# Performance work log

Measured on AMD Instinct MI355X. Metric: run time of the kernel, lower is better.

## Reference

```python
import jax, jax.numpy as jnp
import numpy as np

EMBED = 512
HEADS = 8
HD = EMBED // HEADS  # 64
NCLS = 1
WSIZE = 32
DIL = 2
WIN_LEN = 2 * WSIZE + 1  # 65


def setup_inputs() -> dict:
    key = jax.random.key(0)
    ks = jax.random.split(key, 5)
    B, S = 2, NCLS + 2048
    return {
        "x": jax.random.normal(ks[0], (B, S, EMBED), dtype=jnp.float32),
        "qkv_w": jax.random.normal(ks[1], (3 * EMBED, EMBED), dtype=jnp.float32) * 0.02,
        "qkv_b": jax.random.normal(ks[2], (3 * EMBED,), dtype=jnp.float32) * 0.02,
        "out_w": jax.random.normal(ks[3], (EMBED, EMBED), dtype=jnp.float32) * 0.02,
        "out_b": jax.random.normal(ks[4], (EMBED,), dtype=jnp.float32) * 0.02,
    }


def reference(x, qkv_w, qkv_b, out_w, out_b):
    B, S, E = x.shape
    P = S - NCLS  # patch_len
    scale = HD ** -0.5

    qkv = (x @ qkv_w.T + qkv_b).reshape(B, S, 3, HEADS, HD)
    qkv = qkv.transpose(2, 0, 3, 1, 4)  # (3, B, H, S, d)
    q, k, v = qkv[0], qkv[1], qkv[2]

    q_cls, k_cls, v_cls = q[:, :, :NCLS], k[:, :, :NCLS], v[:, :, :NCLS]
    q_p, k_p, v_p = q[:, :, NCLS:], k[:, :, NCLS:], v[:, :, NCLS:]

    # CLS queries: full attention over all S keys
    s_cls = jnp.einsum('bhqd,bhkd->bhqk', q_cls, k) * scale
    cls_out = jnp.einsum('bhqk,bhkd->bhqd', jax.nn.softmax(s_cls, axis=-1), v)

    # Patch queries: CLS keys + dilated local window
    pad = WSIZE * DIL
    kp = jnp.pad(k_p, ((0, 0), (0, 0), (pad, pad), (0, 0)))
    vp = jnp.pad(v_p, ((0, 0), (0, 0), (pad, pad), (0, 0)))
    idx = jnp.arange(P)[:, None] + jnp.arange(WIN_LEN)[None, :] * DIL  # (P, WL)
    kw = kp[:, :, idx]  # (B, H, P, WL, d)
    vw = vp[:, :, idx]

    sw = jnp.einsum('bhpd,bhpwd->bhpw', q_p, kw) * scale
    pos = jnp.arange(P)[:, None] + (jnp.arange(WIN_LEN) - WSIZE)[None, :] * DIL
    in_bounds = (pos >= 0) & (pos < P)  # (P, WL)
    sw = jnp.where(in_bounds[None, None], sw, -jnp.inf)
    sc = jnp.einsum('bhpd,bhcd->bhpc', q_p, k_cls) * scale

    attn = jax.nn.softmax(jnp.concatenate([sc, sw], axis=-1), axis=-1)
    a_c, a_w = attn[..., :NCLS], attn[..., NCLS:]
    patch_out = (jnp.einsum('bhpc,bhcd->bhpd', a_c, v_cls)
                 + jnp.einsum('bhpw,bhpwd->bhpd', a_w, vw))

    out = jnp.concatenate([cls_out, patch_out], axis=2)  # (B, H, S, d)
    out = out.transpose(0, 2, 1, 3).reshape(B, S, E)
    return out @ out_w.T + out_b
```

## Files before the change

### kernel.cpp

```cpp
#include <hip/hip_runtime.h>
#include <math.h>

#define S_LEN 2049
#define P_LEN 2048
#define EMB 512
#define NH 8
#define HD 64
#define SCALE 0.125f

typedef _Float16 f16x8 __attribute__((ext_vector_type(8)));
typedef float f32x4 __attribute__((ext_vector_type(4)));
typedef unsigned short u16x8 __attribute__((ext_vector_type(8)));

__device__ inline unsigned short f2h(float f) {
  _Float16 h = (_Float16)f;
  return __builtin_bit_cast(unsigned short, h);
}
__device__ inline float h2f(unsigned short u) {
  return (float)__builtin_bit_cast(_Float16, u);
}

__device__ inline float wave_sum64(float v) {
#pragma unroll
  for (int off = 32; off > 0; off >>= 1) v += __shfl_xor(v, off, 64);
  return v;
}

__device__ inline void gld16(const unsigned* g, unsigned* l) {
  __builtin_amdgcn_global_load_lds(
      (const __attribute__((address_space(1))) unsigned*)g,
      (__attribute__((address_space(3))) unsigned*)l, 16, 0, 0);
}

__global__ __launch_bounds__(256) void cvt3_f16(
    const float* __restrict__ s0, unsigned short* __restrict__ d0, int n0,
    const float* __restrict__ s1, unsigned short* __restrict__ d1, int n1,
    const float* __restrict__ s2, unsigned short* __restrict__ d2, int n2) {
  int idx = (blockIdx.x * 256 + threadIdx.x) * 8;
  const float* s;
  unsigned short* d;
  int off;
  if (idx < n0) {
    s = s0; d = d0; off = idx;
  } else if (idx < n0 + n1) {
    s = s1; d = d1; off = idx - n0;
  } else if (idx < n0 + n1 + n2) {
    s = s2; d = d2; off = idx - n0 - n1;
  } else {
    return;
  }
  float4 f0 = *(const float4*)(s + off);
  float4 f1 = *(const float4*)(s + off + 4);
  float ff[8] = {f0.x, f0.y, f0.z, f0.w, f1.x, f1.y, f1.z, f1.w};
  u16x8 vh;
#pragma unroll
  for (int e = 0; e < 8; e++) vh[e] = f2h(ff[e]);
  *(u16x8*)(d + off) = vh;
}

template <int BM, int BN, bool F16OUT>
__global__ __launch_bounds__(256) void gemm_f16(
    const unsigned short* __restrict__ A, const unsigned short* __restrict__ B,
    const float* __restrict__ bias, void* __restrict__ Cv, int M, int N,
    int KP) {
  constexpr int BK = 64;
  __shared__ __align__(16) unsigned short As[BM * BK];
  __shared__ __align__(16) unsigned short Bs[BN * BK];
  const int t = threadIdx.x;
  const int lane = t & 63, wv = t >> 6;
  const int m0 = blockIdx.x * BM, n0 = blockIdx.y * BN;
  constexpr int WM = BM / 2, WN = BN / 2;
  constexpr int RM = WM / 16, RN = WN / 16;
  const int wm = wv & 1, wn = wv >> 1;
  const int lm = lane & 15, lq = lane >> 4;

  f32x4 acc[RM][RN];
#pragma unroll
  for (int i = 0; i < RM; i++)
#pragma unroll
    for (int j = 0; j < RN; j++) acc[i][j] = (f32x4){0.f, 0.f, 0.f, 0.f};

  const int lr = lane >> 3;
  const int lc = (lane & 7) ^ lr;

  const unsigned* aptr[BM / 32];
#pragma unroll
  for (int p = 0; p < BM / 32; p++) {
    int ra = wv * (BM / 4) + p * 8 + lr;
    int gr = m0 + ra;
    gr = gr < M ? gr : M - 1;
    aptr[p] = (const unsigned*)(A + (size_t)gr * KP + lc * 8);
  }
  const unsigned* bptr[BN / 32];
#pragma unroll
  for (int p = 0; p < BN / 32; p++) {
    int rb = wv * (BN / 4) + p * 8 + lr;
    bptr[p] = (const unsigned*)(B + (size_t)(n0 + rb) * KP + lc * 8);
  }

  for (int kt = 0; kt < KP; kt += BK) {
    __syncthreads();
#pragma unroll
    for (int p = 0; p < BM / 32; p++)
      gld16(aptr[p] + (kt >> 1), (unsigned*)&As[(wv * (BM / 4) + p * 8) * BK]);
#pragma unroll
    for (int p = 0; p < BN / 32; p++)
      gld16(bptr[p] + (kt >> 1), (unsigned*)&Bs[(wv * (BN / 4) + p * 8) * BK]);
    __syncthreads();

    f16x8 fa[2][RM], fb[2][RN];
#pragma unroll
    for (int kk = 0; kk < 2; kk++) {
      int ch = ((kk * 4 + lq) ^ (lm & 7)) * 8;
#pragma unroll
      for (int mi = 0; mi < RM; mi++) {
        int ra = wm * WM + mi * 16 + lm;
        fa[kk][mi] = *(const f16x8*)&As[ra * BK + ch];
      }
#pragma unroll
      for (int ni = 0; ni < RN; ni++) {
        int rb = wn * WN + ni * 16 + lm;
        fb[kk][ni] = *(const f16x8*)&Bs[rb * BK + ch];
      }
    }
#pragma unroll
    for (int kk = 0; kk < 2; kk++)
#pragma unroll
      for (int mi = 0; mi < RM; mi++)
#pragma unroll
        for (int ni = 0; ni < RN; ni++)
          acc[mi][ni] = __builtin_amdgcn_mfma_f32_16x16x32_f16(
              fa[kk][mi], fb[kk][ni], acc[mi][ni], 0, 0, 0);
  }

#pragma unroll
  for (int ni = 0; ni < RN; ni++) {
    int n = n0 + wn * WN + ni * 16 + lm;
    float bv = bias[n];
#pragma unroll
    for (int mi = 0; mi < RM; mi++)
#pragma unroll
      for (int r = 0; r < 4; r++) {
        int m = m0 + wm * WM + mi * 16 + lq * 4 + r;
        if (m < M) {
          float val = acc[mi][ni][r] + bv;
          if constexpr (F16OUT)
            ((unsigned short*)Cv)[(size_t)m * N + n] = f2h(val);
          else
            ((float*)Cv)[(size_t)m * N + n] = val;
        }
      }
  }
}

__global__ __launch_bounds__(256) void patch_attn3(
    const unsigned short* __restrict__ qkv16, unsigned short* __restrict__ Aatt,
    const float* __restrict__ Pm, const float* __restrict__ Pl,
    const float* __restrict__ Po) {
  constexpr int LDK = 72;
  constexpr int LDT = 168;
  __shared__ __align__(16) unsigned short Ks[144 * LDK];
  __shared__ __align__(16) unsigned short Vt[64 * LDT];
  __shared__ __align__(16) unsigned short Ps[64 * LDT];

  const int t = threadIdx.x;
  const int lane = t & 63, wv = t >> 6;
  const int lm = lane & 15, lq = lane >> 4;
  const int qb = blockIdx.x;
  const int h = blockIdx.y;
  const int par = blockIdx.z & 1, b = blockIdx.z >> 1;
  const unsigned short* base = qkv16 + (size_t)b * S_LEN * 1536;
  const int qc0 = qb * 64;

  {
    uint4 z = {0, 0, 0, 0};
    if (t < 120) {
      int r = 129 + (t >> 3), c = (t & 7) * 8;
      *(uint4*)&Ks[r * LDK + c] = z;
    }
    {
      int r = t >> 2, c = 128 + (t & 3) * 8;
      *(uint4*)&Vt[r * LDT + c] = z;
    }
    if (t < 128) {
      int r = t >> 1, c = 144 + (t & 1) * 8;
      *(uint4*)&Ps[r * LDT + c] = z;
    }
  }
  __syncthreads();

  {
    int rr = t >> 4;
    int cc = (t & 15) * 4;
#pragma unroll
    for (int pass = 0; pass < 8; pass++) {
      int r = pass * 16 + rr;
      int jc = qc0 - 32 + r;
      uint2 kv = {0, 0};
      if ((unsigned)jc < 1024u)
        kv = *(const uint2*)(base + (size_t)(1 + 2 * jc + par) * 1536 + 512 +
                             h * 64 + cc);
      *(uint2*)&Ks[r * LDK + cc] = kv;
    }
    if (rr == 0)
      *(uint2*)&Ks[128 * LDK + cc] =
          *(const uint2*)(base + 512 + h * 64 + cc);
  }
#pragma unroll
  for (int pass = 0; pass < 4; pass++) {
    int task = pass * 256 + t;
    int jp = task >> 4;
    int d0 = (task & 15) * 4;
    int jc0 = qc0 - 32 + 2 * jp;
    uint2 a = {0, 0}, c = {0, 0};
    if ((unsigned)jc0 < 1024u)
      a = *(const uint2*)(base + (size_t)(1 + 2 * jc0 + par) * 1536 + 1024 +
                          h * 64 + d0);
    if ((unsigned)(jc0 + 1) < 1024u)
      c = *(const uint2*)(base + (size_t)(1 + 2 * (jc0 + 1) + par) * 1536 +
                          1024 + h * 64 + d0);
    *(unsigned*)&Vt[(d0 + 0) * LDT + 2 * jp] = (a.x & 0xffffu) | (c.x << 16);
    *(unsigned*)&Vt[(d0 + 1) * LDT + 2 * jp] = (a.x >> 16) | (c.x & 0xffff0000u);
    *(unsigned*)&Vt[(d0 + 2) * LDT + 2 * jp] = (a.y & 0xffffu) | (c.y << 16);
    *(unsigned*)&Vt[(d0 + 3) * LDT + 2 * jp] = (a.y >> 16) | (c.y & 0xffff0000u);
  }
  if (t < 64) Vt[t * LDT + 128] = base[1024 + h * 64 + t];

  const int qi = wv * 16 + lm;
  const unsigned short* qg =
      base + (size_t)(1 + 2 * (qc0 + qi) + par) * 1536 + h * 64;
  f16x8 qf[2];
  qf[0] = *(const f16x8*)&qg[lq * 8];
  qf[1] = *(const f16x8*)&qg[32 + lq * 8];
  __syncthreads();

  f32x4 s[9];
#pragma unroll
  for (int nt = 0; nt < 9; nt++) s[nt] = (f32x4){0.f, 0.f, 0.f, 0.f};
#pragma unroll
  for (int nt = 0; nt < 9; nt++) {
#pragma unroll
    for (int kk = 0; kk < 2; kk++) {
      f16x8 kb = *(const f16x8*)&Ks[(nt * 16 + lm) * LDK + kk * 32 + lq * 8];
      s[nt] =
          __builtin_amdgcn_mfma_f32_16x16x32_f16(qf[kk], kb, s[nt], 0, 0, 0);
    }
  }

  float L[4];
#pragma unroll
  for (int r = 0; r < 4; r++) {
    int qrow = wv * 16 + lq * 4 + r;
    float sv[9];
    float mx = -1e30f;
#pragma unroll
    for (int nt = 0; nt < 9; nt++) {
      int jl = nt * 16 + lm;
      bool valid =
          (jl == 128) ||
          (jl < 128 && jl >= qrow && jl <= qrow + 64 &&
           (unsigned)(qc0 - 32 + jl) < 1024u);
      sv[nt] = valid ? s[nt][r] * SCALE : -1e30f;
      mx = fmaxf(mx, sv[nt]);
    }
#pragma unroll
    for (int off = 1; off < 16; off <<= 1)
      mx = fmaxf(mx, __shfl_xor(mx, off, 16));
    float l = 0.f;
#pragma unroll
    for (int nt = 0; nt < 9; nt++) {
      float e = __expf(sv[nt] - mx);
      l += e;
      Ps[qrow * LDT + nt * 16 + lm] = f2h(e);
    }
#pragma unroll
    for (int off = 1; off < 16; off <<= 1) l += __shfl_xor(l, off, 16);
    L[r] = l;
  }
  __syncthreads();

  f32x4 oa[4];
#pragma unroll
  for (int nt = 0; nt < 4; nt++) oa[nt] = (f32x4){0.f, 0.f, 0.f, 0.f};
#pragma unroll
  for (int kc = 0; kc < 5; kc++) {
    f16x8 pa = *(const f16x8*)&Ps[(wv * 16 + lm) * LDT + kc * 32 + lq * 8];
#pragma unroll
    for (int nt = 0; nt < 4; nt++) {
      f16x8 vb = *(const f16x8*)&Vt[(nt * 16 + lm) * LDT + kc * 32 + lq * 8];
      oa[nt] = __builtin_amdgcn_mfma_f32_16x16x32_f16(pa, vb, oa[nt], 0, 0, 0);
    }
  }

#pragma unroll
  for (int r = 0; r < 4; r++) {
    float inv = 1.f / L[r];
    int qrow = wv * 16 + lq * 4 + r;
    int pp = 2 * (qc0 + qrow) + par;
    unsigned short* ab = Aatt + ((size_t)b * S_LEN + 1 + pp) * 512 + h * 64;
#pragma unroll
    for (int nt = 0; nt < 4; nt++) ab[nt * 16 + lm] = f2h(oa[nt][r] * inv);
  }

  if (qb == 0 && par == 0 && t < 64) {
    float m = -1e30f, l = 0.f, o = 0.f;
    for (int ck = 0; ck < 32; ck++) {
      int idx = (b * NH + h) * 32 + ck;
      float mc = Pm[idx];
      float lc = Pl[idx];
      float oc = Po[(size_t)idx * 64 + t];
      float mn = fmaxf(m, mc);
      float e0 = __expf(m - mn);
      float e1 = __expf(mc - mn);
      l = l * e0 + lc * e1;
      o = o * e0 + oc * e1;
      m = mn;
    }
    Aatt[(size_t)b * S_LEN * 512 + h * HD + t] = f2h(o / l);
  }
}

__global__ __launch_bounds__(256) void cls_part_k(
    const unsigned short* __restrict__ qkv16, float* __restrict__ Pm,
    float* __restrict__ Pl, float* __restrict__ Po) {
  const int lane = threadIdx.x & 63;
  const int wv = threadIdx.x >> 6;
  const int ck = blockIdx.x;
  const int h = blockIdx.y;
  const int b = blockIdx.z;
  const unsigned short* base = qkv16 + (size_t)b * S_LEN * 1536;
  float qd = h2f(base[h * 64 + lane]) * SCALE;

  int c0 = ck * 64;
  int cend = (ck == 31) ? S_LEN : c0 + 64;

  float m = -1e30f, l = 0.f, o = 0.f;
  for (int j = c0 + wv; j < cend; j += 4) {
    const unsigned short* krow = base + (size_t)j * 1536 + 512 + h * 64;
    float kv = h2f(krow[lane]);
    float vv = h2f(krow[512 + lane]);
    float s = wave_sum64(qd * kv);
    float mn = fmaxf(m, s);
    float e0 = __expf(m - mn);
    float e1 = __expf(s - mn);
    l = l * e0 + e1;
    o = o * e0 + e1 * vv;
    m = mn;
  }

  __shared__ float sm[4], sl[4], so[4][64];
  if (lane == 0) {
    sm[wv] = m;
    sl[wv] = l;
  }
  so[wv][lane] = o;
  __syncthreads();
  if (wv == 0) {
    float M = -1e30f;
#pragma unroll
    for (int i = 0; i < 4; i++) M = fmaxf(M, sm[i]);
    float L = 0.f, O = 0.f;
#pragma unroll
    for (int i = 0; i < 4; i++) {
      float c = __expf(sm[i] - M);
      L += sl[i] * c;
      O += so[i][lane] * c;
    }
    int idx = (b * NH + h) * 32 + ck;
    if (lane == 0) {
      Pm[idx] = M;
      Pl[idx] = L;
    }
    Po[(size_t)idx * 64 + lane] = O;
  }
}

extern "C" void kernel_launch(void* const* d_in, const int* in_sizes, int n_in,
                              void* d_out, int out_size, void* d_ws,
                              size_t ws_size, hipStream_t stream) {
  const float* x = (const float*)d_in[0];
  const float* qkv_w = (const float*)d_in[1];
  const float* qkv_b = (const float*)d_in[2];
  const float* out_w = (const float*)d_in[3];
  const float* out_b = (const float*)d_in[4];
  float* out = (float*)d_out;

  const int M = 2 * S_LEN;

  float* cls_pm = (float*)d_ws;
  float* cls_pl = cls_pm + 512;
  float* cls_po = cls_pl + 512;
  unsigned short* Xp = (unsigned short*)(cls_po + 32768);
  unsigned short* Wq = Xp + (size_t)M * 512;
  unsigned short* Wo = Wq + (size_t)1536 * 512;
  unsigned short* Aatt = Wo + (size_t)512 * 512;
  unsigned short* qkv16 = Aatt + (size_t)M * 512;

  const int n0 = M * EMB;
  const int n1 = 1536 * EMB;
  const int n2 = EMB * EMB;
  int cvt_blocks = ((n0 + n1 + n2) / 8 + 255) / 256;
  cvt3_f16<<<cvt_blocks, 256, 0, stream>>>(x, Xp, n0, qkv_w, Wq, n1, out_w, Wo,
                                           n2);

  dim3 gq((M + 63) / 64, 1536 / 128);
  gemm_f16<64, 128, true><<<gq, 256, 0, stream>>>(Xp, Wq, qkv_b, qkv16, M,
                                                  1536, 512);

  cls_part_k<<<dim3(32, NH, 2), 256, 0, stream>>>(qkv16, cls_pm, cls_pl,
                                                  cls_po);
  patch_attn3<<<dim3(16, NH, 4), 256, 0, stream>>>(qkv16, Aatt, cls_pm, cls_pl,
                                                   cls_po);

  dim3 go((M + 63) / 64, EMB / 64);
  gemm_f16<64, 64, false><<<go, 256, 0, stream>>>(Aatt, Wo, out_b, out, M, EMB,
                                                  512);
}
```

Measured before the change: 118.4 us.

## Fold CLS full attention into patch attention kernel as extra blocks

Removes the separate CLS partial-softmax kernel and its combine step. Extra blocks with qb==0 in the patch attention grid now compute the CLS query's full attention over all keys. Each wave processes 8 keys at a time with 8-element vector loads and an online softmax, and the results are merged across waves in shared memory. This drops one kernel launch and the global round trip for the partial results. In exchange, the CLS work is done serially by 16 blocks, which can lengthen the tail of the attention kernel.

```diff
diff --git a/kernel.cpp b/kernel.cpp
--- a/kernel.cpp
+++ b/kernel.cpp
@@ -18,12 +18,6 @@
 }
 __device__ inline float h2f(unsigned short u) {
   return (float)__builtin_bit_cast(_Float16, u);
-}
-
-__device__ inline float wave_sum64(float v) {
-#pragma unroll
-  for (int off = 32; off > 0; off >>= 1) v += __shfl_xor(v, off, 64);
-  return v;
 }
 
 __device__ inline void gld16(const unsigned* g, unsigned* l) {
@@ -154,9 +148,8 @@
 }
 
 __global__ __launch_bounds__(256) void patch_attn3(
-    const unsigned short* __restrict__ qkv16, unsigned short* __restrict__ Aatt,
-    const float* __restrict__ Pm, const float* __restrict__ Pl,
-    const float* __restrict__ Po) {
+    const unsigned short* __restrict__ qkv16,
+    unsigned short* __restrict__ Aatt) {
   constexpr int LDK = 72;
   constexpr int LDT = 168;
   __shared__ __align__(16) unsigned short Ks[144 * LDK];
@@ -170,7 +163,85 @@
   const int h = blockIdx.y;
   const int par = blockIdx.z & 1, b = blockIdx.z >> 1;
   const unsigned short* base = qkv16 + (size_t)b * S_LEN * 1536;
-  const int qc0 = qb * 64;
+
+  if (qb == 0) {
+    if (par == 1) return;
+    const int kidx = lane >> 3, c = lane & 7, d0 = c * 8;
+    float qv[8];
+    {
+      f16x8 qh = *(const f16x8*)(base + h * 64 + d0);
+#pragma unroll
+      for (int i = 0; i < 8; i++) qv[i] = (float)qh[i] * SCALE;
+    }
+    float m = -1e30f, l = 0.f, o[8];
+#pragma unroll
+    for (int i = 0; i < 8; i++) o[i] = 0.f;
+
+    for (int it = 0; it < 65; it++) {
+      int j = it * 32 + wv * 8 + kidx;
+      bool valid = j < S_LEN;
+      f16x8 kh, vh;
+      if (valid) {
+        const unsigned short* row = base + (size_t)j * 1536 + 512 + h * 64;
+        kh = *(const f16x8*)(row + d0);
+        vh = *(const f16x8*)(row + 512 + d0);
+      }
+      float dp = 0.f;
+      if (valid) {
+#pragma unroll
+        for (int i = 0; i < 8; i++) dp += qv[i] * (float)kh[i];
+      }
+#pragma unroll
+      for (int off = 1; off < 8; off <<= 1) dp += __shfl_xor(dp, off, 64);
+      float s = valid ? dp : -1e30f;
+      float cmax = s;
+#pragma unroll
+      for (int off = 8; off < 64; off <<= 1)
+        cmax = fmaxf(cmax, __shfl_xor(cmax, off, 64));
+      float mn = fmaxf(m, cmax);
+      float sc = __expf(m - mn);
+      float e = valid ? __expf(s - mn) : 0.f;
+      float esum = e;
+#pragma unroll
+      for (int off = 8; off < 64; off <<= 1) esum += __shfl_xor(esum, off, 64);
+      l = l * sc + esum;
+#pragma unroll
+      for (int i = 0; i < 8; i++)
+        o[i] = o[i] * sc + (valid ? e * (float)vh[i] : 0.f);
+      m = mn;
+    }
+#pragma unroll
+    for (int i = 0; i < 8; i++) {
+#pragma unroll
+      for (int off = 8; off < 64; off <<= 1) o[i] += __shfl_xor(o[i], off, 64);
+    }
+    float* SF = (float*)Ks;
+    if (kidx == 0) {
+#pragma unroll
+      for (int i = 0; i < 8; i++) SF[wv * 64 + d0 + i] = o[i];
+    }
+    if (lane == 0) {
+      SF[256 + wv] = m;
+      SF[260 + wv] = l;
+    }
+    __syncthreads();
+    if (t < 64) {
+      float M = -1e30f;
+#pragma unroll
+      for (int i = 0; i < 4; i++) M = fmaxf(M, SF[256 + i]);
+      float L = 0.f, O = 0.f;
+#pragma unroll
+      for (int i = 0; i < 4; i++) {
+        float cexp = __expf(SF[256 + i] - M);
+        L += SF[260 + i] * cexp;
+        O += SF[i * 64 + t] * cexp;
+      }
+      Aatt[(size_t)b * S_LEN * 512 + h * HD + t] = f2h(O / L);
+    }
+    return;
+  }
+
+  const int qc0 = (qb - 1) * 64;
 
   {
     uint4 z = {0, 0, 0, 0};
@@ -301,78 +372,6 @@
 #pragma unroll
     for (int nt = 0; nt < 4; nt++) ab[nt * 16 + lm] = f2h(oa[nt][r] * inv);
   }
-
-  if (qb == 0 && par == 0 && t < 64) {
-    float m = -1e30f, l = 0.f, o = 0.f;
-    for (int ck = 0; ck < 32; ck++) {
-      int idx = (b * NH + h) * 32 + ck;
-      float mc = Pm[idx];
-      float lc = Pl[idx];
-      float oc = Po[(size_t)idx * 64 + t];
-      float mn = fmaxf(m, mc);
-      float e0 = __expf(m - mn);
-      float e1 = __expf(mc - mn);
-      l = l * e0 + lc * e1;
-      o = o * e0 + oc * e1;
-      m = mn;
-    }
-    Aatt[(size_t)b * S_LEN * 512 + h * HD + t] = f2h(o / l);
-  }
-}
-
-__global__ __launch_bounds__(256) void cls_part_k(
-    const unsigned short* __restrict__ qkv16, float* __restrict__ Pm,
-    float* __restrict__ Pl, float* __restrict__ Po) {
-  const int lane = threadIdx.x & 63;
-  const int wv = threadIdx.x >> 6;
-  const int ck = blockIdx.x;
-  const int h = blockIdx.y;
-  const int b = blockIdx.z;
-  const unsigned short* base = qkv16 + (size_t)b * S_LEN * 1536;
-  float qd = h2f(base[h * 64 + lane]) * SCALE;
-
-  int c0 = ck * 64;
-  int cend = (ck == 31) ? S_LEN : c0 + 64;
-
-  float m = -1e30f, l = 0.f, o = 0.f;
-  for (int j = c0 + wv; j < cend; j += 4) {
-    const unsigned short* krow = base + (size_t)j * 1536 + 512 + h * 64;
-    float kv = h2f(krow[lane]);
-    float vv = h2f(krow[512 + lane]);
-    float s = wave_sum64(qd * kv);
-    float mn = fmaxf(m, s);
-    float e0 = __expf(m - mn);
-    float e1 = __expf(s - mn);
-    l = l * e0 + e1;
-    o = o * e0 + e1 * vv;
-    m = mn;
-  }
-
-  __shared__ float sm[4], sl[4], so[4][64];
-  if (lane == 0) {
-    sm[wv] = m;
-    sl[wv] = l;
-  }
-  so[wv][lane] = o;
-  __syncthreads();
-  if (wv == 0) {
-    float M = -1e30f;
-#pragma unroll
-    for (int i = 0; i < 4; i++) M = fmaxf(M, sm[i]);
-    float L = 0.f, O = 0.f;
-#pragma unroll
-    for (int i = 0; i < 4; i++) {
-      float c = __expf(sm[i] - M);
-      L += sl[i] * c;
-      O += so[i][lane] * c;
-    }
-    int idx = (b * NH + h) * 32 + ck;
-    if (lane == 0) {
-      Pm[idx] = M;
-      Pl[idx] = L;
-    }
-    Po[(size_t)idx * 64 + lane] = O;
-  }
 }
 
 extern "C" void kernel_launch(void* const* d_in, const int* in_sizes, int n_in,
@@ -387,10 +386,7 @@
 
   const int M = 2 * S_LEN;
 
-  float* cls_pm = (float*)d_ws;
-  float* cls_pl = cls_pm + 512;
-  float* cls_po = cls_pl + 512;
-  unsigned short* Xp = (unsigned short*)(cls_po + 32768);
+  unsigned short* Xp = (unsigned short*)((float*)d_ws + 33792);
   unsigned short* Wq = Xp + (size_t)M * 512;
   unsigned short* Wo = Wq + (size_t)1536 * 512;
   unsigned short* Aatt = Wo + (size_t)512 * 512;
@@ -407,10 +403,7 @@
   gemm_f16<64, 128, true><<<gq, 256, 0, stream>>>(Xp, Wq, qkv_b, qkv16, M,
                                                   1536, 512);
 
-  cls_part_k<<<dim3(32, NH, 2), 256, 0, stream>>>(qkv16, cls_pm, cls_pl,
-                                                  cls_po);
-  patch_attn3<<<dim3(16, NH, 4), 256, 0, stream>>>(qkv16, Aatt, cls_pm, cls_pl,
-                                                   cls_po);
+  patch_attn3<<<dim3(17, NH, 4), 256, 0, stream>>>(qkv16, Aatt);
 
   dim3 go((M + 63) / 64, EMB / 64);
   gemm_f16<64, 64, false><<<go, 256, 0, stream>>>(Aatt, Wo, out_b, out, M, EMB,
```

Measured after the change: 143.4 us. 21.1% more time.
